# Performance work log

Measured on AMD Instinct MI355X. Metric: run time of the kernel, lower is better.

The kernel has to match this reference:

```python
import jax, jax.numpy as jnp
import numpy as np

N1, N2, K = 262144, 65536, 16   # dense points, coarse points, knn neighbors
CIN, COUT = 64, 64              # in_planes, out_planes
EPS = 1e-5


def bn(x, g, b, m, v):
    # eval-mode BatchNorm1d with learned affine and running stats
    return (x - m) * jax.lax.rsqrt(v + EPS) * g + b


def setup_inputs() -> dict:
    key = jax.random.key(0)
    ks = jax.random.split(key, 32)
    u = lambda k, *s: jax.random.normal(k, s, jnp.float32)
    lin = lambda k, o, i: jax.random.normal(k, (o, i), jnp.float32) / np.float32(np.sqrt(i))
    inp = dict(
        p1=u(ks[0], N1, 3), p2=u(ks[1], N2, 3),
        x1=u(ks[2], N1, COUT), x2=u(ks[3], N2, CIN),
        knn_idx=jax.random.randint(ks[4], (N2, K), 0, N1),
        # linear1: Linear(COUT,COUT) + BN + ReLU
        w1=lin(ks[5], COUT, COUT), b1=0.01 * u(ks[6], COUT),
        g1=jnp.ones(COUT), be1=jnp.zeros(COUT),
        m1=0.1 * u(ks[7], COUT), v1=jax.random.uniform(ks[8], (COUT,), minval=0.5, maxval=1.5),
        # linear2: Linear(CIN,COUT) + BN + ReLU
        w2=lin(ks[9], COUT, CIN), b2=0.01 * u(ks[10], COUT),
        g2=jnp.ones(COUT), be2=jnp.zeros(COUT),
        m2=0.1 * u(ks[11], COUT), v2=jax.random.uniform(ks[12], (COUT,), minval=0.5, maxval=1.5),
        # channel_shrinker: Linear(CIN+3,CIN) + BN + ReLU + Linear(CIN,1)
        ws1=lin(ks[13], CIN, CIN + 3), bs1=0.01 * u(ks[14], CIN),
        gs=jnp.ones(CIN), bes=jnp.zeros(CIN),
        ms=0.1 * u(ks[15], CIN), vs=jax.random.uniform(ks[16], (CIN,), minval=0.5, maxval=1.5),
        ws2=lin(ks[17], 1, CIN), bs2=0.01 * u(ks[18], 1),
    )
    return inp


def reference(p1, p2, x1, x2, knn_idx,
              w1, b1, g1, be1, m1, v1,
              w2, b2, g2, be2, m2, v2,
              ws1, bs1, gs, bes, ms, vs, ws2, bs2):
    idx = knn_idx.reshape(-1)                                   # [M] = [N2*K], indices into p1
    # relative position of each knn neighbor to its coarse query point
    p_r = p1[idx].reshape(N2, K, 3) - p2[:, None, :]            # [N2,K,3]
    x2k = jnp.concatenate(
        [p_r, jnp.broadcast_to(x2[:, None, :], (N2, K, CIN))], axis=-1
    ).reshape(N2 * K, CIN + 3)                                  # [M, CIN+3]
    # channel_shrinker MLP -> scalar logit per (coarse, neighbor) pair
    h = jax.nn.relu(bn(x2k @ ws1.T + bs1, gs, bes, ms, vs))     # [M, CIN]
    logit = (h @ ws2.T + bs2)[:, 0]                             # [M]
    # scatter_softmax over variable in-degree groups keyed by dense point idx
    gmax = jax.lax.stop_gradient(jax.ops.segment_max(logit, idx, num_segments=N1))
    e = jnp.exp(logit - gmax[idx])
    denom = jax.ops.segment_sum(e, idx, num_segments=N1)
    prob = e / denom[idx]                                       # [M]
    # linear2(x2), broadcast over K neighbors, weight, scatter-sum to dense points
    up_feat = jax.nn.relu(bn(x2 @ w2.T + b2, g2, be2, m2, v2))  # [N2, COUT]
    weighted = (up_feat[:, None, :] * prob.reshape(N2, K, 1)).reshape(N2 * K, COUT)
    up = jax.ops.segment_sum(weighted, idx, num_segments=N1)    # [N1, COUT]
    # skip branch: linear1(x1)
    y1 = jax.nn.relu(bn(x1 @ w1.T + b1, g1, be1, m1, v1))       # [N1, COUT]
    return y1 + up
```

## Files before the change

kernel.cpp:

```cpp
#include <hip/hip_runtime.h>

#define CN1 262144
#define CN2 65536
#define CK  16
#define CM  (CN2*CK)

typedef unsigned short u16;
typedef unsigned char  u8;
typedef unsigned int   u32;
typedef float f32x4 __attribute__((ext_vector_type(4)));

__device__ __forceinline__ float b2f(u16 h) {
    union { u32 u; float f; } v; v.u = ((u32)h) << 16; return v.f;
}
__device__ __forceinline__ u16 f2b(float f) {
    union { float f; u32 u; } v; v.f = f;
    u32 lsb = (v.u >> 16) & 1u;
    return (u16)((v.u + 0x7FFFu + lsb) >> 16);
}
__device__ __forceinline__ float u2f(u32 u) {
    union { u32 u; float f; } v; v.u = u; return v.f;
}
__device__ __forceinline__ u32 f2u(float f) {
    union { float f; u32 u; } v; v.f = f; return v.u;
}

#define W_POS   0
#define W_FT    256
#define W_AS    12544
#define W_BS    12608
#define W_WS2   12672
#define W_A2    12736
#define W_B2    12800
#define W_A1    12864
#define W_B1    12928
#define W_BS2   12992
#define W_MODE  13000
#define W_W1T   13056
#define W_W2T   17152
#define W_JP    21248

__device__ __forceinline__ float ldv(const void* p, size_t i, int bf) {
    return bf ? b2f(((const u16*)p)[i]) : ((const float*)p)[i];
}

#define FMA4(A, Wv) \
    (A).x = fmaf(xv_, (Wv).x, (A).x); (A).y = fmaf(xv_, (Wv).y, (A).y); \
    (A).z = fmaf(xv_, (Wv).z, (A).z); (A).w = fmaf(xv_, (Wv).w, (A).w);

#define DECL_ACC16 \
    f32x4 A0={0,0,0,0},A1={0,0,0,0},A2={0,0,0,0},A3={0,0,0,0}, \
          A4={0,0,0,0},A5={0,0,0,0},A6={0,0,0,0},A7={0,0,0,0}, \
          A8={0,0,0,0},A9={0,0,0,0},A10={0,0,0,0},A11={0,0,0,0}, \
          A12={0,0,0,0},A13={0,0,0,0},A14={0,0,0,0},A15={0,0,0,0};

#define WSTEP16(wt, ivar, xval) { \
    float xv_ = (xval); \
    const f32x4* wr_ = (const f32x4*)((wt) + ((size_t)(ivar) << 6)); \
    FMA4(A0, wr_[0])   FMA4(A1, wr_[1])   FMA4(A2, wr_[2])   FMA4(A3, wr_[3]) \
    FMA4(A4, wr_[4])   FMA4(A5, wr_[5])   FMA4(A6, wr_[6])   FMA4(A7, wr_[7]) \
    FMA4(A8, wr_[8])   FMA4(A9, wr_[9])   FMA4(A10,wr_[10])  FMA4(A11,wr_[11]) \
    FMA4(A12,wr_[12])  FMA4(A13,wr_[13])  FMA4(A14,wr_[14])  FMA4(A15,wr_[15]) }

#define GEMV64T(bf, xrow_f, xrow_u4, wt) \
    if (bf) { \
        const uint4* xu_ = (xrow_u4); \
        _Pragma("unroll 2") \
        for (int ii_ = 0; ii_ < 8; ++ii_) { \
            uint4 xc_ = xu_[ii_]; \
            WSTEP16(wt, ii_*8+0, b2f((u16)(xc_.x & 0xffffu))) \
            WSTEP16(wt, ii_*8+1, b2f((u16)(xc_.x >> 16))) \
            WSTEP16(wt, ii_*8+2, b2f((u16)(xc_.y & 0xffffu))) \
            WSTEP16(wt, ii_*8+3, b2f((u16)(xc_.y >> 16))) \
            WSTEP16(wt, ii_*8+4, b2f((u16)(xc_.z & 0xffffu))) \
            WSTEP16(wt, ii_*8+5, b2f((u16)(xc_.z >> 16))) \
            WSTEP16(wt, ii_*8+6, b2f((u16)(xc_.w & 0xffffu))) \
            WSTEP16(wt, ii_*8+7, b2f((u16)(xc_.w >> 16))) \
        } \
    } else { \
        const float4* xf_ = (xrow_f); \
        _Pragma("unroll 2") \
        for (int ii_ = 0; ii_ < 8; ++ii_) { \
            float4 xa_ = xf_[2*ii_], xb_ = xf_[2*ii_+1]; \
            WSTEP16(wt, ii_*8+0, xa_.x) WSTEP16(wt, ii_*8+1, xa_.y) \
            WSTEP16(wt, ii_*8+2, xa_.z) WSTEP16(wt, ii_*8+3, xa_.w) \
            WSTEP16(wt, ii_*8+4, xb_.x) WSTEP16(wt, ii_*8+5, xb_.y) \
            WSTEP16(wt, ii_*8+6, xb_.z) WSTEP16(wt, ii_*8+7, xb_.w) \
        } \
    }

#define DECL_ACC8 \
    f32x4 A0={0,0,0,0},A1={0,0,0,0},A2={0,0,0,0},A3={0,0,0,0}, \
          A4={0,0,0,0},A5={0,0,0,0},A6={0,0,0,0},A7={0,0,0,0};

#define WSTEP8(wtco, ivar, xval) { \
    float xv_ = (xval); \
    const f32x4* wr_ = (const f32x4*)((wtco) + ((size_t)(ivar) << 6)); \
    FMA4(A0, wr_[0])  FMA4(A1, wr_[1])  FMA4(A2, wr_[2])  FMA4(A3, wr_[3]) \
    FMA4(A4, wr_[4])  FMA4(A5, wr_[5])  FMA4(A6, wr_[6])  FMA4(A7, wr_[7]) }

#define GEMV32T(bf, xrow_f, xrow_u4, wtco) \
    if (bf) { \
        const uint4* xu_ = (xrow_u4); \
        _Pragma("unroll 2") \
        for (int ii_ = 0; ii_ < 8; ++ii_) { \
            uint4 xc_ = xu_[ii_]; \
            WSTEP8(wtco, ii_*8+0, b2f((u16)(xc_.x & 0xffffu))) \
            WSTEP8(wtco, ii_*8+1, b2f((u16)(xc_.x >> 16))) \
            WSTEP8(wtco, ii_*8+2, b2f((u16)(xc_.y & 0xffffu))) \
            WSTEP8(wtco, ii_*8+3, b2f((u16)(xc_.y >> 16))) \
            WSTEP8(wtco, ii_*8+4, b2f((u16)(xc_.z & 0xffffu))) \
            WSTEP8(wtco, ii_*8+5, b2f((u16)(xc_.z >> 16))) \
            WSTEP8(wtco, ii_*8+6, b2f((u16)(xc_.w & 0xffffu))) \
            WSTEP8(wtco, ii_*8+7, b2f((u16)(xc_.w >> 16))) \
        } \
    } else { \
        const float4* xf_ = (xrow_f); \
        _Pragma("unroll 2") \
        for (int ii_ = 0; ii_ < 8; ++ii_) { \
            float4 xa_ = xf_[2*ii_], xb_ = xf_[2*ii_+1]; \
            WSTEP8(wtco, ii_*8+0, xa_.x) WSTEP8(wtco, ii_*8+1, xa_.y) \
            WSTEP8(wtco, ii_*8+2, xa_.z) WSTEP8(wtco, ii_*8+3, xa_.w) \
            WSTEP8(wtco, ii_*8+4, xb_.x) WSTEP8(wtco, ii_*8+5, xb_.y) \
            WSTEP8(wtco, ii_*8+6, xb_.z) WSTEP8(wtco, ii_*8+7, xb_.w) \
        } \
    }

#define BNR1(A, av, bv) \
    (A).x = fmaxf(fmaf((A).x,(av).x,(bv).x),0.f); \
    (A).y = fmaxf(fmaf((A).y,(av).y,(bv).y),0.f); \
    (A).z = fmaxf(fmaf((A).z,(av).z,(bv).z),0.f); \
    (A).w = fmaxf(fmaf((A).w,(av).w,(bv).w),0.f);
#define BNR16(aBase, bBase) { \
    const f32x4* av_ = (const f32x4*)(aBase); \
    const f32x4* bv_ = (const f32x4*)(bBase); \
    BNR1(A0,av_[0],bv_[0])   BNR1(A1,av_[1],bv_[1]) \
    BNR1(A2,av_[2],bv_[2])   BNR1(A3,av_[3],bv_[3]) \
    BNR1(A4,av_[4],bv_[4])   BNR1(A5,av_[5],bv_[5]) \
    BNR1(A6,av_[6],bv_[6])   BNR1(A7,av_[7],bv_[7]) \
    BNR1(A8,av_[8],bv_[8])   BNR1(A9,av_[9],bv_[9]) \
    BNR1(A10,av_[10],bv_[10]) BNR1(A11,av_[11],bv_[11]) \
    BNR1(A12,av_[12],bv_[12]) BNR1(A13,av_[13],bv_[13]) \
    BNR1(A14,av_[14],bv_[14]) BNR1(A15,av_[15],bv_[15]) }
#define BNR8(aBase, bBase) { \
    const f32x4* av_ = (const f32x4*)(aBase); \
    const f32x4* bv_ = (const f32x4*)(bBase); \
    BNR1(A0,av_[0],bv_[0]) BNR1(A1,av_[1],bv_[1]) \
    BNR1(A2,av_[2],bv_[2]) BNR1(A3,av_[3],bv_[3]) \
    BNR1(A4,av_[4],bv_[4]) BNR1(A5,av_[5],bv_[5]) \
    BNR1(A6,av_[6],bv_[6]) BNR1(A7,av_[7],bv_[7]) }

#define UFQ(q, AL, AH) { uint4 u_ = ufr_[q]; \
    (AL).x = fmaf(pe_, b2f((u16)(u_.x & 0xffffu)), (AL).x); \
    (AL).y = fmaf(pe_, b2f((u16)(u_.x >> 16)),     (AL).y); \
    (AL).z = fmaf(pe_, b2f((u16)(u_.y & 0xffffu)), (AL).z); \
    (AL).w = fmaf(pe_, b2f((u16)(u_.y >> 16)),     (AL).w); \
    (AH).x = fmaf(pe_, b2f((u16)(u_.z & 0xffffu)), (AH).x); \
    (AH).y = fmaf(pe_, b2f((u16)(u_.z >> 16)),     (AH).y); \
    (AH).z = fmaf(pe_, b2f((u16)(u_.w & 0xffffu)), (AH).z); \
    (AH).w = fmaf(pe_, b2f((u16)(u_.w >> 16)),     (AH).w); }

#define STQ(q, AL, AH, dst) { uint4 o_; \
    o_.x = (u32)f2b((AL).x) | ((u32)f2b((AL).y) << 16); \
    o_.y = (u32)f2b((AL).z) | ((u32)f2b((AL).w) << 16); \
    o_.z = (u32)f2b((AH).x) | ((u32)f2b((AH).y) << 16); \
    o_.w = (u32)f2b((AH).z) | ((u32)f2b((AH).w) << 16); \
    ((uint4*)(dst))[q] = o_; }
#define STORE_BF16V(dst) \
    STQ(0,A0,A1,dst)  STQ(1,A2,A3,dst)  STQ(2,A4,A5,dst)  STQ(3,A6,A7,dst) \
    STQ(4,A8,A9,dst)  STQ(5,A10,A11,dst) STQ(6,A12,A13,dst) STQ(7,A14,A15,dst)
#define STORE_F3216(dst) { f32x4* ov_ = (f32x4*)(dst); \
    ov_[0]=A0;  ov_[1]=A1;  ov_[2]=A2;  ov_[3]=A3; \
    ov_[4]=A4;  ov_[5]=A5;  ov_[6]=A6;  ov_[7]=A7; \
    ov_[8]=A8;  ov_[9]=A9;  ov_[10]=A10;ov_[11]=A11; \
    ov_[12]=A12;ov_[13]=A13;ov_[14]=A14;ov_[15]=A15; }
#define STORE_BF8V(dst) \
    STQ(0,A0,A1,dst) STQ(1,A2,A3,dst) STQ(2,A4,A5,dst) STQ(3,A6,A7,dst)
#define STORE_F328(dst) { f32x4* ov_ = (f32x4*)(dst); \
    ov_[0]=A0; ov_[1]=A1; ov_[2]=A2; ov_[3]=A3; \
    ov_[4]=A4; ov_[5]=A5; ov_[6]=A6; ov_[7]=A7; }

__global__ __launch_bounds__(256) void k_prep(
    const void* __restrict__ w1,  const void* __restrict__ b1,  const void* __restrict__ g1,
    const void* __restrict__ be1, const void* __restrict__ m1,  const void* __restrict__ v1,
    const void* __restrict__ w2,  const void* __restrict__ b2,  const void* __restrict__ g2,
    const void* __restrict__ be2, const void* __restrict__ m2,  const void* __restrict__ v2,
    const void* __restrict__ ws1, const void* __restrict__ bs1, const void* __restrict__ gs,
    const void* __restrict__ bes, const void* __restrict__ ms,  const void* __restrict__ vs,
    const void* __restrict__ ws2, const void* __restrict__ bs2, float* __restrict__ wb,
    u32* __restrict__ offsets, u32* __restrict__ cursor)
{
    int b = blockIdx.x;
    int tid = threadIdx.x;
    if (b > 0) {
        offsets[(b - 1) * 256 + tid] = 0u;
        if (b == 1 && tid == 0) *cursor = 0u;
        return;
    }

    u32 w0 = ((const u32*)g1)[0];
    int bf = (w0 != 0x3F800000u) ? 1 : 0;

    for (int t = tid; t < 64*64; t += 256) {
        int i = t >> 6, c = t & 63;
        wb[W_FT  + t] = ldv(ws1, (size_t)c*67 + 3 + i, bf);
        wb[W_W1T + t] = ldv(w1,  (size_t)c*64 + i, bf);
        wb[W_W2T + t] = ldv(w2,  (size_t)c*64 + i, bf);
    }
    for (int t = tid; t < 64*3; t += 256) {
        int j = t / 3, k = t % 3;
        wb[W_POS + t] = ldv(ws1, (size_t)j*67 + k, bf);
    }
    if (tid < 64) {
        float as = ldv(gs, tid, bf) * rsqrtf(ldv(vs, tid, bf) + 1e-5f);
        float bs = (ldv(bs1, tid, bf) - ldv(ms, tid, bf)) * as + ldv(bes, tid, bf);
        float wc = ldv(ws2, tid, bf);
        wb[W_AS + tid] = as;
        wb[W_BS + tid] = bs;
        wb[W_WS2 + tid] = wc;
        float a2 = ldv(g2, tid, bf) * rsqrtf(ldv(v2, tid, bf) + 1e-5f);
        wb[W_A2 + tid] = a2;
        wb[W_B2 + tid] = (ldv(b2, tid, bf) - ldv(m2, tid, bf)) * a2 + ldv(be2, tid, bf);
        float a1 = ldv(g1, tid, bf) * rsqrtf(ldv(v1, tid, bf) + 1e-5f);
        wb[W_A1 + tid] = a1;
        wb[W_B1 + tid] = (ldv(b1, tid, bf) - ldv(m1, tid, bf)) * a1 + ldv(be1, tid, bf);
        wb[W_JP + tid*8 + 0] = ldv(ws1, (size_t)tid*67 + 0, bf);
        wb[W_JP + tid*8 + 1] = ldv(ws1, (size_t)tid*67 + 1, bf);
        wb[W_JP + tid*8 + 2] = ldv(ws1, (size_t)tid*67 + 2, bf);
        wb[W_JP + tid*8 + 3] = as;
        wb[W_JP + tid*8 + 4] = bs;
        wb[W_JP + tid*8 + 5] = wc;
        wb[W_JP + tid*8 + 6] = 0.f;
        wb[W_JP + tid*8 + 7] = 0.f;
    }
    if (tid == 0) {
        wb[W_BS2] = ldv(bs2, 0, bf);
        ((u32*)wb)[W_MODE] = (u32)bf;
    }
}

__global__ __launch_bounds__(256, 8) void k_coarse2(
    const void* __restrict__ x2, const int* __restrict__ knn,
    const float* __restrict__ wb,
    float* __restrict__ dots, u16* __restrict__ upfeat,
    u32* __restrict__ offsets, u8* __restrict__ rank8)
{
    int bf   = (int)((const u32*)wb)[W_MODE];
    int tid  = threadIdx.x;
    int role = blockIdx.x & 1;
    int lane = tid & 63;
    int co   = __builtin_amdgcn_readfirstlane(((tid >> 6) & 1) << 5);
    int n2   = (blockIdx.x >> 1) * 128 + (tid >> 7) * 64 + lane;
    const float4* xf = (const float4*)((const float*)x2 + (size_t)n2 * 64);
    const uint4*  xu = (const uint4*)((const u16*)x2 + (size_t)n2 * 64);

    if (role == 0) {
        if (co == 0) {
            const int4* kv = (const int4*)(knn + (size_t)n2 * 16);
            u32 rw0, rw1, rw2, rw3;
            #define CNT4(T, RW) { \
                u32 r0_ = atomicAdd(&offsets[(T).x & (CN1-1)], 1u); \
                u32 r1_ = atomicAdd(&offsets[(T).y & (CN1-1)], 1u); \
                u32 r2_ = atomicAdd(&offsets[(T).z & (CN1-1)], 1u); \
                u32 r3_ = atomicAdd(&offsets[(T).w & (CN1-1)], 1u); \
                RW = (r0_ & 0xffu) | ((r1_ & 0xffu) << 8) | \
                     ((r2_ & 0xffu) << 16) | ((r3_ & 0xffu) << 24); }
            int4 t0 = kv[0]; CNT4(t0, rw0)
            int4 t1 = kv[1]; CNT4(t1, rw1)
            int4 t2 = kv[2]; CNT4(t2, rw2)
            int4 t3 = kv[3]; CNT4(t3, rw3)
            #undef CNT4
            uint4 rv; rv.x = rw0; rv.y = rw1; rv.z = rw2; rv.w = rw3;
            ((uint4*)rank8)[n2] = rv;
        }
        DECL_ACC8
        GEMV32T(bf, xf, xu, wb + W_FT + co)
        STORE_F328(dots + (size_t)n2 * 64 + co)
    } else {
        DECL_ACC8
        GEMV32T(bf, xf, xu, wb + W_W2T + co)
        BNR8(wb + W_A2 + co, wb + W_B2 + co)
        STORE_BF8V(upfeat + (size_t)n2 * 64 + co)
    }
}

__global__ __launch_bounds__(256) void k_scan(
    u32* __restrict__ offsets, u32* __restrict__ cursor)
{
    __shared__ u32 s[256];
    __shared__ u32 base;
    int t = threadIdx.x;
    int i = blockIdx.x * 256 + t;
    u32 v = offsets[i];
    s[t] = v; __syncthreads();
    for (int off = 1; off < 256; off <<= 1) {
        u32 add = (t >= off) ? s[t-off] : 0u;
        __syncthreads();
        s[t] += add;
        __syncthreads();
    }
    u32 inc = s[t];
    if (t == 255) base = atomicAdd(cursor, inc);
    __syncthreads();
    offsets[i] = ((base + inc - v) << 6) | (v & 63u);
}

#define LSTEP(j, dv) { f32x4 pa_ = jp[2*(j)], pb_ = jp[2*(j)+1]; \
    float pre_ = fmaf(prz, pa_.z, fmaf(pry, pa_.y, fmaf(prx, pa_.x, (dv)))); \
    float h_ = fmaxf(fmaf(pre_, pa_.w, pb_.x), 0.f); \
    lg = fmaf(h_, pb_.y, lg); }

__global__ __launch_bounds__(256) void k_logit_scatter(
    const void* __restrict__ p1, const void* __restrict__ p2,
    const int* __restrict__ knn, const float* __restrict__ wb,
    const float* __restrict__ dots, const u8* __restrict__ rank8,
    const u32* __restrict__ offsets, uint2* __restrict__ epair)
{
    int bf = (int)((const u32*)wb)[W_MODE];
    int m  = blockIdx.x * 256 + threadIdx.x;
    int n2 = m >> 4;

    int idx = knn[m] & (CN1-1);
    u32 rk  = (u32)rank8[m];
    u32 pos = ((offsets[idx] >> 6) + rk) & (CM-1);

    float prx = ldv(p1, (size_t)idx*3+0, bf) - ldv(p2, (size_t)n2*3+0, bf);
    float pry = ldv(p1, (size_t)idx*3+1, bf) - ldv(p2, (size_t)n2*3+1, bf);
    float prz = ldv(p1, (size_t)idx*3+2, bf) - ldv(p2, (size_t)n2*3+2, bf);

    const f32x4*  jp  = (const f32x4*)(wb + W_JP);
    const float4* dr4 = (const float4*)(dots + (size_t)n2 * 64);
    float lg = 0.f;
    #pragma unroll 4
    for (int jq = 0; jq < 16; ++jq) {
        float4 d4 = dr4[jq];
        LSTEP(jq*4+0, d4.x) LSTEP(jq*4+1, d4.y)
        LSTEP(jq*4+2, d4.z) LSTEP(jq*4+3, d4.w)
    }
    uint2 e;
    e.x = (u32)m;
    e.y = f2u(lg + wb[W_BS2]);
    epair[pos] = e;
}

__global__ __launch_bounds__(256, 4) void k_dense(
    const void* __restrict__ x1, const float* __restrict__ wb,
    const uint2* __restrict__ epair, const u16* __restrict__ upfeat,
    const u32* __restrict__ offsets, void* __restrict__ out)
{
    int bf = (int)((const u32*)wb)[W_MODE];
    int n1 = blockIdx.x * 256 + threadIdx.x;

    u32 pk = offsets[n1];
    int d = (int)(pk & 63u);
    int start = (int)(pk >> 6);

    float mxv = -3.0e38f, s = 0.f;
    for (int e = 0; e < d; ++e) {
        float l = u2f(epair[(u32)(start + e) & (CM-1)].y);
        float mnew = fmaxf(mxv, l);
        s = fmaf(s, __expf(mxv - mnew), __expf(l - mnew));
        mxv = mnew;
    }
    float inv = (d > 0) ? (1.f / s) : 0.f;

    DECL_ACC16
    GEMV64T(bf, (const float4*)((const float*)x1 + (size_t)n1 * 64),
                (const uint4*)((const u16*)x1 + (size_t)n1 * 64),
                wb + W_W1T)
    BNR16(wb + W_A1, wb + W_B1)

    for (int e = 0; e < d; ++e) {
        uint2 t = epair[(u32)(start + e) & (CM-1)];
        float pe_ = __expf(u2f(t.y) - mxv) * inv;
        u32 m = t.x & (CM-1);
        const uint4* ufr_ = (const uint4*)(upfeat + (size_t)(m >> 4) * 64);
        UFQ(0,A0,A1)   UFQ(1,A2,A3)   UFQ(2,A4,A5)   UFQ(3,A6,A7)
        UFQ(4,A8,A9)   UFQ(5,A10,A11) UFQ(6,A12,A13) UFQ(7,A14,A15)
    }

    if (bf) { u16* orow = (u16*)out + (size_t)n1 * 64; STORE_BF16V(orow) }
    else    { STORE_F3216((float*)out + (size_t)n1 * 64) }
}

extern "C" void kernel_launch(void* const* d_in, const int* in_sizes, int n_in,
                              void* d_out, int out_size, void* d_ws, size_t ws_size,
                              hipStream_t stream)
{
    (void)in_sizes; (void)n_in; (void)out_size; (void)ws_size;
    const void* p1   = d_in[0];
    const void* p2   = d_in[1];
    const void* x1   = d_in[2];
    const void* x2   = d_in[3];
    const int*  knn  = (const int*)d_in[4];
    const void* w1   = d_in[5];
    const void* b1   = d_in[6];
    const void* g1   = d_in[7];
    const void* be1  = d_in[8];
    const void* m1   = d_in[9];
    const void* v1   = d_in[10];
    const void* w2   = d_in[11];
    const void* b2   = d_in[12];
    const void* g2   = d_in[13];
    const void* be2  = d_in[14];
    const void* m2   = d_in[15];
    const void* v2   = d_in[16];
    const void* ws1  = d_in[17];
    const void* bs1  = d_in[18];
    const void* gs   = d_in[19];
    const void* bes  = d_in[20];
    const void* ms   = d_in[21];
    const void* vs   = d_in[22];
    const void* ws2w = d_in[23];
    const void* bs2  = d_in[24];

    char* ws = (char*)d_ws;
    float* wb      = (float*)(ws);
    uint2* epair   = (uint2*)(ws + ((size_t)1  << 20));
    u16*   upfeat  = (u16*)  (ws + ((size_t)9  << 20));
    u32*   offsets = (u32*)  (ws + ((size_t)17 << 20));
    u32*   cursor  = (u32*)  (ws + ((size_t)18 << 20));
    u8*    rank8   = (u8*)   (ws + ((size_t)19 << 20));
    float* dots    = (float*)d_out;

    k_prep          <<<1 + CN1/256, 256, 0, stream>>>(w1,b1,g1,be1,m1,v1,
                                                      w2,b2,g2,be2,m2,v2,
                                                      ws1,bs1,gs,bes,ms,vs,
                                                      ws2w, bs2, wb, offsets, cursor);
    k_coarse2       <<<2*(CN2/128), 256, 0, stream>>>(x2, knn, wb, dots, upfeat,
                                                      offsets, rank8);
    k_scan          <<<CN1/256,     256, 0, stream>>>(offsets, cursor);
    k_logit_scatter <<<CM/256,      256, 0, stream>>>(p1, p2, knn, wb, dots,
                                                      rank8, offsets, epair);
    k_dense         <<<CN1/256,     256, 0, stream>>>(x1, wb, epair, upfeat,
                                                      offsets, d_out);
}
```

Before: 194.8 us.

## Split each dense point across two lanes in k_dense and combine via shuffles

Each dense point is now handled by a pair of lanes. The lanes split the in-degree edges between them for both the online softmax and the weighted upfeat accumulation, then merge their partial max, sum and accumulators with xor shuffles. The skip-branch GEMV is computed redundantly by both lanes and halved before accumulation, and each lane stores half of the output row. The aim is to cut the serial per-thread edge loop and raise memory-level parallelism on the gathers, at the cost of doubling the GEMV work and adding shuffles. Launch bounds are raised to 8 waves to push occupancy.

```diff
diff --git a/kernel.cpp b/kernel.cpp
--- a/kernel.cpp
+++ b/kernel.cpp
@@ -149,6 +149,18 @@
     BNR1(A2,av_[2],bv_[2]) BNR1(A3,av_[3],bv_[3]) \
     BNR1(A4,av_[4],bv_[4]) BNR1(A5,av_[5],bv_[5]) \
     BNR1(A6,av_[6],bv_[6]) BNR1(A7,av_[7],bv_[7]) }
+
+#define HALF16 \
+    A0*=0.5f; A1*=0.5f; A2*=0.5f; A3*=0.5f; A4*=0.5f; A5*=0.5f; A6*=0.5f; A7*=0.5f; \
+    A8*=0.5f; A9*=0.5f; A10*=0.5f; A11*=0.5f; A12*=0.5f; A13*=0.5f; A14*=0.5f; A15*=0.5f;
+
+#define BFLY1(A) { \
+    (A).x += __shfl_xor((A).x, 1, 64); (A).y += __shfl_xor((A).y, 1, 64); \
+    (A).z += __shfl_xor((A).z, 1, 64); (A).w += __shfl_xor((A).w, 1, 64); }
+#define BFLY16 \
+    BFLY1(A0)  BFLY1(A1)  BFLY1(A2)  BFLY1(A3)  BFLY1(A4)  BFLY1(A5) \
+    BFLY1(A6)  BFLY1(A7)  BFLY1(A8)  BFLY1(A9)  BFLY1(A10) BFLY1(A11) \
+    BFLY1(A12) BFLY1(A13) BFLY1(A14) BFLY1(A15)
 
 #define UFQ(q, AL, AH) { uint4 u_ = ufr_[q]; \
     (AL).x = fmaf(pe_, b2f((u16)(u_.x & 0xffffu)), (AL).x); \
@@ -343,24 +355,33 @@
     epair[pos] = e;
 }
 
-__global__ __launch_bounds__(256, 4) void k_dense(
+__global__ __launch_bounds__(256, 8) void k_dense(
     const void* __restrict__ x1, const float* __restrict__ wb,
     const uint2* __restrict__ epair, const u16* __restrict__ upfeat,
     const u32* __restrict__ offsets, void* __restrict__ out)
 {
-    int bf = (int)((const u32*)wb)[W_MODE];
-    int n1 = blockIdx.x * 256 + threadIdx.x;
+    int bf  = (int)((const u32*)wb)[W_MODE];
+    int tid = threadIdx.x;
+    int h   = tid & 1;
+    int n1  = blockIdx.x * 128 + (tid >> 1);
 
     u32 pk = offsets[n1];
     int d = (int)(pk & 63u);
     int start = (int)(pk >> 6);
 
     float mxv = -3.0e38f, s = 0.f;
-    for (int e = 0; e < d; ++e) {
+    for (int e = h; e < d; e += 2) {
         float l = u2f(epair[(u32)(start + e) & (CM-1)].y);
         float mnew = fmaxf(mxv, l);
         s = fmaf(s, __expf(mxv - mnew), __expf(l - mnew));
         mxv = mnew;
+    }
+    {
+        float mxo = __shfl_xor(mxv, 1, 64);
+        float so  = __shfl_xor(s,   1, 64);
+        float mxt = fmaxf(mxv, mxo);
+        s = s * __expf(mxv - mxt) + so * __expf(mxo - mxt);
+        mxv = mxt;
     }
     float inv = (d > 0) ? (1.f / s) : 0.f;
 
@@ -369,8 +390,9 @@
                 (const uint4*)((const u16*)x1 + (size_t)n1 * 64),
                 wb + W_W1T)
     BNR16(wb + W_A1, wb + W_B1)
-
-    for (int e = 0; e < d; ++e) {
+    HALF16
+
+    for (int e = h; e < d; e += 2) {
         uint2 t = epair[(u32)(start + e) & (CM-1)];
         float pe_ = __expf(u2f(t.y) - mxv) * inv;
         u32 m = t.x & (CM-1);
@@ -379,8 +401,19 @@
         UFQ(4,A8,A9)   UFQ(5,A10,A11) UFQ(6,A12,A13) UFQ(7,A14,A15)
     }
 
-    if (bf) { u16* orow = (u16*)out + (size_t)n1 * 64; STORE_BF16V(orow) }
-    else    { STORE_F3216((float*)out + (size_t)n1 * 64) }
+    BFLY16
+
+    if (bf) {
+        u16* orow = (u16*)out + (size_t)n1 * 64;
+        if (h == 0) { STQ(0,A0,A1,orow) STQ(1,A2,A3,orow) STQ(2,A4,A5,orow) STQ(3,A6,A7,orow) }
+        else        { STQ(4,A8,A9,orow) STQ(5,A10,A11,orow) STQ(6,A12,A13,orow) STQ(7,A14,A15,orow) }
+    } else {
+        f32x4* ov_ = (f32x4*)((float*)out + (size_t)n1 * 64);
+        if (h == 0) { ov_[0]=A0; ov_[1]=A1; ov_[2]=A2; ov_[3]=A3;
+                      ov_[4]=A4; ov_[5]=A5; ov_[6]=A6; ov_[7]=A7; }
+        else        { ov_[8]=A8;  ov_[9]=A9;  ov_[10]=A10; ov_[11]=A11;
+                      ov_[12]=A12; ov_[13]=A13; ov_[14]=A14; ov_[15]=A15; }
+    }
 }
 
 extern "C" void kernel_launch(void* const* d_in, const int* in_sizes, int n_in,
@@ -432,6 +465,6 @@
     k_scan          <<<CN1/256,     256, 0, stream>>>(offsets, cursor);
     k_logit_scatter <<<CM/256,      256, 0, stream>>>(p1, p2, knn, wb, dots,
                                                       rank8, offsets, epair);
-    k_dense         <<<CN1/256,     256, 0, stream>>>(x1, wb, epair, upfeat,
+    k_dense         <<<CN1/128,     256, 0, stream>>>(x1, wb, epair, upfeat,
                                                       offsets, d_out);
 }
```

Result: slower. 696.3 us (+257.5%).
